# Kernel tuning notes

Hardware: AMD Instinct MI355X
Metric: run time of the kernel (lower is better)

## Reference

```python
import jax, jax.numpy as jnp
import numpy as np

H = 16  # n_heads

def setup_inputs() -> dict:
    key = jax.random.key(0)
    ks = jax.random.split(key, 12)
    B, L, S, D = 4, 2048, 2048, 1024
    E = D // H  # d_keys = d_values = 64
    s = 1.0 / np.sqrt(D)
    inp = {
        "queries": jax.random.normal(ks[0], (B, L, D), jnp.float32),
        "keys": jax.random.normal(ks[1], (B, S, D), jnp.float32),
        "values": jax.random.normal(ks[2], (B, S, D), jnp.float32),
        # causal boolean mask: True = masked out
        "attn_mask": jnp.triu(jnp.ones((L, S), jnp.bool_), k=1)[None, None],
        "Wq": jax.random.normal(ks[3], (H * E, D), jnp.float32) * s,
        "bq": jnp.zeros((H * E,), jnp.float32),
        "Wk": jax.random.normal(ks[4], (H * E, D), jnp.float32) * s,
        "bk": jnp.zeros((H * E,), jnp.float32),
        "Wv": jax.random.normal(ks[5], (H * E, D), jnp.float32) * s,
        "bv": jnp.zeros((H * E,), jnp.float32),
        "Wo": jax.random.normal(ks[6], (D, H * E), jnp.float32) * s,
        "bo": jnp.zeros((D,), jnp.float32),
    }
    return inp


def reference(queries, keys, values, attn_mask, Wq, bq, Wk, bk, Wv, bv, Wo, bo):
    B, L, D = queries.shape
    S = keys.shape[1]
    E = Wq.shape[0] // H
    # QKV projections + head split: (B, L/S, H, E)
    q = (queries @ Wq.T + bq).reshape(B, L, H, E)
    k = (keys @ Wk.T + bk).reshape(B, S, H, E)
    v = (values @ Wv.T + bv).reshape(B, S, H, E)
    scale = 1.0 / jnp.sqrt(jnp.asarray(E, q.dtype))
    scores = jnp.einsum("blhe,bshe->bhls", q, k) * scale  # (B,H,L,S)
    scores = jnp.where(attn_mask, jnp.asarray(-jnp.inf, scores.dtype), scores)
    A = jax.nn.softmax(scores, axis=-1)
    out = jnp.einsum("bhls,bshe->blhe", A, v).reshape(B, L, H * E)
    return out @ Wo.T + bo
```

## Files before the change

### kernel.cpp

```cpp
#include <hip/hip_runtime.h>
#include <hip/hip_bf16.h>

typedef float f32x4 __attribute__((ext_vector_type(4)));
typedef short s16x8 __attribute__((ext_vector_type(8)));
typedef short s16x4 __attribute__((ext_vector_type(4)));
typedef unsigned short u16;

#define H_ 16
#define E_ 64
#define D_ 1024
#define L_ 2048
#define NQT 32
#define SCL2E 0.18033688011f

__device__ __forceinline__ u16 f2bf(float f) {
  union { float f; unsigned u; } v; v.f = f;
  unsigned u = v.u;
  u += 0x7fffu + ((u >> 16) & 1u);
  return (u16)(u >> 16);
}

__device__ __forceinline__ unsigned pkbf(float a, float b) {
  unsigned r;
  asm("v_cvt_pk_bf16_f32 %0, %1, %2" : "=v"(r) : "v"(a), "v"(b));
  return r;
}

__device__ __forceinline__ void gld16(const u16* g, u16* l) {
  __builtin_amdgcn_global_load_lds((const __attribute__((address_space(1))) void*)g,
                                   (__attribute__((address_space(3))) void*)l, 16, 0, 0);
}

__global__ __launch_bounds__(256) void cvtall(const float* __restrict__ q,
                                              const float* __restrict__ k,
                                              const float* __restrict__ v,
                                              const float* __restrict__ w0,
                                              const float* __restrict__ w1,
                                              const float* __restrict__ w2,
                                              const float* __restrict__ w3,
                                              u16* __restrict__ qd,
                                              u16* __restrict__ kd,
                                              u16* __restrict__ vd,
                                              u16* __restrict__ d0,
                                              u16* __restrict__ d1,
                                              u16* __restrict__ d2,
                                              u16* __restrict__ d3) {
  const int b = blockIdx.x;
  const float* src; u16* dst; float s = 1.0f; size_t off;
  if (b < 12288) {
    const int y = b >> 12, bx = b & 4095;
    src = y == 0 ? q : (y == 1 ? k : v);
    dst = y == 0 ? qd : (y == 1 ? kd : vd);
    off = ((size_t)bx * 256 + threadIdx.x) * 8;
  } else {
    const int b2 = b - 12288, y = b2 >> 9, bx = b2 & 511;
    src = y == 0 ? w0 : (y == 1 ? w1 : (y == 2 ? w2 : w3));
    dst = y == 0 ? d0 : (y == 1 ? d1 : (y == 2 ? d2 : d3));
    if (y == 0) s = SCL2E;
    off = ((size_t)bx * 256 + threadIdx.x) * 8;
  }
  const f32x4 a = *(const f32x4*)(src + off);
  const f32x4 c = *(const f32x4*)(src + off + 4);
  s16x8 r;
#pragma unroll
  for (int j = 0; j < 4; ++j) { r[j] = (short)f2bf(a[j] * s); r[j + 4] = (short)f2bf(c[j] * s); }
  *(s16x8*)(dst + off) = r;
}

template<int PERMUTE>
__global__ __launch_bounds__(256) void gemm_lds(const u16* __restrict__ A,
                                                const u16* __restrict__ W,
                                                const float* __restrict__ bias,
                                                void* __restrict__ outp,
                                                int M, int N, int K, float bsc)
{
  __shared__ __align__(16) u16 As[2][128][64];
  __shared__ __align__(16) u16 Bs[2][128][64];
  const int tid = threadIdx.x;
  const int m0 = blockIdx.y * 128, n0 = blockIdx.x * 128;
  const int w = tid >> 6, lane = tid & 63, g = lane >> 4, li = lane & 15;
  const int wr = w >> 1, wc = w & 1;

  int sOff[4];
#pragma unroll
  for (int j = 0; j < 4; ++j) {
    const int s = (w * 4 + j) * 64 + lane;
    const int row = s >> 3, c8 = s & 7;
    sOff[j] = row * K + ((c8 ^ (row & 7)) * 8);
  }

  f32x4 acc[4][4];
#pragma unroll
  for (int i = 0; i < 4; ++i)
#pragma unroll
    for (int j = 0; j < 4; ++j) acc[i][j] = (f32x4){0.f, 0.f, 0.f, 0.f};

  const u16* Abase = A + (size_t)m0 * K;
  const u16* Wbase = W + (size_t)n0 * K;
  const int swz = li & 7;

  auto STAGE = [&](int k0, int bf) {
#pragma unroll
    for (int j = 0; j < 4; ++j) {
      gld16(Abase + k0 + sOff[j], &As[bf][(w * 4 + j) * 8][0]);
      gld16(Wbase + k0 + sOff[j], &Bs[bf][(w * 4 + j) * 8][0]);
    }
  };

  STAGE(0, 0);
  __syncthreads();
  int buf = 0;
  for (int k0 = 0; k0 < K; k0 += 64) {
    if (k0 + 64 < K) STAGE(k0 + 64, buf ^ 1);

    s16x8 a[2][4], b[2][4];
#pragma unroll
    for (int kk = 0; kk < 2; ++kk) {
      const int cg = ((kk * 4 + g) ^ swz) * 8;
#pragma unroll
      for (int mi = 0; mi < 4; ++mi) a[kk][mi] = *(const s16x8*)&As[buf][wr * 64 + mi * 16 + li][cg];
#pragma unroll
      for (int ni = 0; ni < 4; ++ni) b[kk][ni] = *(const s16x8*)&Bs[buf][wc * 64 + ni * 16 + li][cg];
    }
#pragma unroll
    for (int kk = 0; kk < 2; ++kk)
#pragma unroll
      for (int mi = 0; mi < 4; ++mi)
#pragma unroll
        for (int ni = 0; ni < 4; ++ni)
          acc[mi][ni] = __builtin_amdgcn_mfma_f32_16x16x32_bf16(a[kk][mi], b[kk][ni], acc[mi][ni], 0, 0, 0);

    __syncthreads();
    buf ^= 1;
  }

#pragma unroll
  for (int mi = 0; mi < 4; ++mi) {
#pragma unroll
    for (int ni = 0; ni < 4; ++ni) {
      const int row = m0 + wr * 64 + mi * 16 + g * 4;
      const int col = n0 + wc * 64 + ni * 16 + li;
      const float bv = bias[col] * bsc;
      if (PERMUTE == 2) {
        s16x4 pk;
#pragma unroll
        for (int r = 0; r < 4; ++r) pk[r] = (short)f2bf(acc[mi][ni][r] + bv);
        const int bb = row >> 11, lq = row & (L_ - 1);
        const int hh = col >> 6, e = col & (E_ - 1);
        *(s16x4*)&((u16*)outp)[(((size_t)bb * H_ + hh) * E_ + e) * L_ + lq] = pk;
      } else {
#pragma unroll
        for (int r = 0; r < 4; ++r) {
          const float v = acc[mi][ni][r] + bv;
          const int rr = row + r;
          if (PERMUTE == 1) {
            const int bb = rr >> 11, lq = rr & (L_ - 1);
            const int hh = col >> 6, e = col & (E_ - 1);
            ((u16*)outp)[(((size_t)bb * H_ + hh) * L_ + lq) * E_ + e] = f2bf(v);
          } else {
            ((float*)outp)[(size_t)rr * N + col] = v;
          }
        }
      }
    }
  }
}

template<int A_BF16, int PERMUTE>
__global__ __launch_bounds__(256) void gemm_bt(const void* __restrict__ Aptr,
                                               const float* __restrict__ W,
                                               const float* __restrict__ bias,
                                               void* __restrict__ outp,
                                               int M, int N, int K, float osc)
{
  __shared__ __align__(16) short As[2][128][40];
  __shared__ __align__(16) short Bs[2][128][40];
  const int tid = threadIdx.x;
  const int m0 = blockIdx.y * 128, n0 = blockIdx.x * 128;
  const int w = tid >> 6, lane = tid & 63, g = lane >> 4, li = lane & 15;
  const int wr = w >> 1, wc = w & 1;

  f32x4 acc[4][4];
#pragma unroll
  for (int i = 0; i < 4; ++i)
#pragma unroll
    for (int j = 0; j < 4; ++j) acc[i][j] = (f32x4){0.f, 0.f, 0.f, 0.f};

  f32x4 ra0[2], ra1[2];
  s16x8 rab[2];
  f32x4 rb0[2], rb1[2];

  auto LOAD = [&](int k0) {
#pragma unroll
    for (int p = 0; p < 2; ++p) {
      const int c = p * 256 + tid, row = c >> 2, kc = (c & 3) * 8;
      if (A_BF16) {
        rab[p] = *(const s16x8*)((const u16*)Aptr + (size_t)(m0 + row) * K + k0 + kc);
      } else {
        const float* ap = (const float*)Aptr + (size_t)(m0 + row) * K + k0 + kc;
        ra0[p] = *(const f32x4*)ap; ra1[p] = *(const f32x4*)(ap + 4);
      }
      const float* wp = W + (size_t)(n0 + row) * K + k0 + kc;
      rb0[p] = *(const f32x4*)wp; rb1[p] = *(const f32x4*)(wp + 4);
    }
  };
  auto WRITE = [&](int buf) {
#pragma unroll
    for (int p = 0; p < 2; ++p) {
      const int c = p * 256 + tid, row = c >> 2, kc = (c & 3) * 8;
      if (A_BF16) {
        *(s16x8*)&As[buf][row][kc] = rab[p];
      } else {
        s16x8 r;
#pragma unroll
        for (int j = 0; j < 4; ++j) { r[j] = (short)f2bf(ra0[p][j]); r[j + 4] = (short)f2bf(ra1[p][j]); }
        *(s16x8*)&As[buf][row][kc] = r;
      }
      s16x8 rb;
#pragma unroll
      for (int j = 0; j < 4; ++j) { rb[j] = (short)f2bf(rb0[p][j]); rb[j + 4] = (short)f2bf(rb1[p][j]); }
      *(s16x8*)&Bs[buf][row][kc] = rb;
    }
  };

  LOAD(0); WRITE(0);
  __syncthreads();
  int cur = 0;
  for (int k0 = 0; k0 < K; k0 += 32) {
    const bool more = (k0 + 32 < K);
    if (more) LOAD(k0 + 32);

    s16x8 a[4], b[4];
#pragma unroll
    for (int mi = 0; mi < 4; ++mi) a[mi] = *(const s16x8*)&As[cur][wr * 64 + mi * 16 + li][g * 8];
#pragma unroll
    for (int ni = 0; ni < 4; ++ni) b[ni] = *(const s16x8*)&Bs[cur][wc * 64 + ni * 16 + li][g * 8];
#pragma unroll
    for (int mi = 0; mi < 4; ++mi)
#pragma unroll
      for (int ni = 0; ni < 4; ++ni)
        acc[mi][ni] = __builtin_amdgcn_mfma_f32_16x16x32_bf16(a[mi], b[ni], acc[mi][ni], 0, 0, 0);

    if (more) { WRITE(cur ^ 1); __syncthreads(); }
    cur ^= 1;
  }

#pragma unroll
  for (int mi = 0; mi < 4; ++mi) {
#pragma unroll
    for (int ni = 0; ni < 4; ++ni) {
      const int row = m0 + wr * 64 + mi * 16 + g * 4;
      const int col = n0 + wc * 64 + ni * 16 + li;
      const float bv = bias[col];
      if (PERMUTE == 2) {
        s16x4 pk;
#pragma unroll
        for (int r = 0; r < 4; ++r) pk[r] = (short)f2bf((acc[mi][ni][r] + bv) * osc);
        const int bb = row >> 11, lq = row & (L_ - 1);
        const int hh = col >> 6, e = col & (E_ - 1);
        *(s16x4*)&((u16*)outp)[(((size_t)bb * H_ + hh) * E_ + e) * L_ + lq] = pk;
      } else {
#pragma unroll
        for (int r = 0; r < 4; ++r) {
          const float v = (acc[mi][ni][r] + bv) * osc;
          const int rr = row + r;
          if (PERMUTE == 1) {
            const int bb = rr >> 11, lq = rr & (L_ - 1);
            const int hh = col >> 6, e = col & (E_ - 1);
            ((u16*)outp)[(((size_t)bb * H_ + hh) * L_ + lq) * E_ + e] = f2bf(v);
          } else {
            ((float*)outp)[(size_t)rr * N + col] = v;
          }
        }
      }
    }
  }
}

__global__ __launch_bounds__(256) void attn_kernel(const u16* __restrict__ qp,
                                                   const u16* __restrict__ kp,
                                                   const u16* __restrict__ vtp,
                                                   u16* __restrict__ op)
{
  __shared__ __align__(16) u16 Ks[2][4096];
  __shared__ __align__(16) u16 Vs[2][4096];
  const int tid = threadIdx.x;
  const unsigned wgid = blockIdx.x;
  const int bh = (wgid & 7) * 8 + ((wgid >> 3) & 7);
  const int qb = NQT - 1 - (int)(wgid >> 6);
  const int w = tid >> 6, lane = tid & 63, g = lane >> 4, li = lane & 15;
  const size_t base  = (size_t)bh * L_ * E_;
  const size_t baseT = (size_t)bh * E_ * L_;
  const int bb = bh >> 4, hh = bh & 15;
  const int qbase = qb * 64;

  const u16* qr = qp + base + (size_t)(qbase + w * 16 + li) * E_;
  const s16x8 qa0 = *(const s16x8*)(qr + g * 8);
  const s16x8 qa1 = *(const s16x8*)(qr + 32 + g * 8);

  f32x4 o[4];
  float m_run = -1e30f, l_run = 0.f;
#pragma unroll
  for (int nc = 0; nc < 4; ++nc) o[nc] = (f32x4){0.f, 0.f, 0.f, 0.f};

  int kSrc[2], vSrc[2];
#pragma unroll
  for (int j = 0; j < 2; ++j) {
    const int s = (w * 2 + j) * 64 + lane;
    const int row = s >> 3;
    const int c8 = (s & 7) ^ ((row & 3) | (((row >> 3) & 1) << 2));
    kSrc[j] = row * E_ + c8 * 8;
    vSrc[j] = row * L_ + c8 * 8;
  }
  auto stage = [&](int t, int buf) {
    const int kvb = t * 64;
#pragma unroll
    for (int j = 0; j < 2; ++j) {
      gld16(kp + base + (size_t)kvb * E_ + kSrc[j], &Ks[buf][(w * 2 + j) * 512]);
      gld16(vtp + baseT + kvb + vSrc[j],            &Vs[buf][(w * 2 + j) * 512]);
    }
  };

  const int swzk = li & 7;
  const int swzv = (li & 3) | (((li >> 3) & 1) << 2);
  int kRd[8], vRd[8];
#pragma unroll
  for (int inst = 0; inst < 4; ++inst) {
    const int bs = (32 * (inst >> 1) + 4 * (inst & 1) + 8 * (li >> 2) + (li & 3)) * 8;
    kRd[inst * 2]     = (bs + (g ^ swzk)) * 8;
    kRd[inst * 2 + 1] = (bs + ((g + 4) ^ swzk)) * 8;
  }
#pragma unroll
  for (int nc = 0; nc < 4; ++nc) {
    const int es = (nc * 16 + li) * 8;
    vRd[nc * 2]     = (es + (g ^ swzv)) * 8;
    vRd[nc * 2 + 1] = (es + ((g + 4) ^ swzv)) * 8;
  }

  stage(0, 0);
  __syncthreads();
  int buf = 0;
  for (int t = 0; t <= qb; ++t) {
    const bool more = (t < qb);
    if (more) stage(t + 1, buf ^ 1);

    s16x8 kf[8];
#pragma unroll
    for (int i = 0; i < 8; ++i) kf[i] = *(const s16x8*)&Ks[buf][kRd[i]];
    f32x4 p[4];
#pragma unroll
    for (int inst = 0; inst < 4; ++inst) {
      f32x4 sf = (f32x4){0.f, 0.f, 0.f, 0.f};
      sf = __builtin_amdgcn_mfma_f32_16x16x32_bf16(kf[inst * 2],     qa0, sf, 0, 0, 0);
      sf = __builtin_amdgcn_mfma_f32_16x16x32_bf16(kf[inst * 2 + 1], qa1, sf, 0, 0, 0);
      p[inst] = sf;
    }
    if (t == qb) {
      const int qrow = qbase + w * 16 + li;
      const int kvb = t * 64;
#pragma unroll
      for (int inst = 0; inst < 4; ++inst)
#pragma unroll
        for (int r = 0; r < 4; ++r)
          if (kvb + 32 * (inst >> 1) + 8 * g + 4 * (inst & 1) + r > qrow) p[inst][r] = -1e30f;
    }

    s16x8 vf[8];
#pragma unroll
    for (int i = 0; i < 8; ++i) vf[i] = *(const s16x8*)&Vs[buf][vRd[i]];

    {
      float m0_ = fmaxf(fmaxf(p[0][0], p[0][1]), fmaxf(p[0][2], p[0][3]));
      float m1_ = fmaxf(fmaxf(p[1][0], p[1][1]), fmaxf(p[1][2], p[1][3]));
      float m2_ = fmaxf(fmaxf(p[2][0], p[2][1]), fmaxf(p[2][2], p[2][3]));
      float m3_ = fmaxf(fmaxf(p[3][0], p[3][1]), fmaxf(p[3][2], p[3][3]));
      const float mx16 = fmaxf(fmaxf(m0_, m1_), fmaxf(m2_, m3_));
      if (__any(mx16 > m_run + 8.0f)) {
        float mx = fmaxf(mx16, __shfl_xor(mx16, 16));
        mx = fmaxf(mx, __shfl_xor(mx, 32));
        const float mn = fmaxf(m_run, mx);
        const float alpha = __builtin_amdgcn_exp2f(m_run - mn);
        m_run = mn;
        l_run *= alpha;
#pragma unroll
        for (int nc = 0; nc < 4; ++nc)
#pragma unroll
          for (int r = 0; r < 4; ++r) o[nc][r] *= alpha;
      }
    }
    unsigned pk[8];
    float rs = 0.f;
#pragma unroll
    for (int inst = 0; inst < 4; ++inst) {
      const float e0 = __builtin_amdgcn_exp2f(p[inst][0] - m_run);
      const float e1 = __builtin_amdgcn_exp2f(p[inst][1] - m_run);
      const float e2 = __builtin_amdgcn_exp2f(p[inst][2] - m_run);
      const float e3 = __builtin_amdgcn_exp2f(p[inst][3] - m_run);
      rs += (e0 + e1) + (e2 + e3);
      pk[inst * 2]     = pkbf(e0, e1);
      pk[inst * 2 + 1] = pkbf(e2, e3);
    }
    l_run += rs;

    union { s16x8 v; unsigned u[4]; } A0, A1;
    A0.u[0] = pk[0]; A0.u[1] = pk[1]; A0.u[2] = pk[2]; A0.u[3] = pk[3];
    A1.u[0] = pk[4]; A1.u[1] = pk[5]; A1.u[2] = pk[6]; A1.u[3] = pk[7];
#pragma unroll
    for (int nc = 0; nc < 4; ++nc) {
      o[nc] = __builtin_amdgcn_mfma_f32_16x16x32_bf16(vf[nc * 2],     A0.v, o[nc], 0, 0, 0);
      o[nc] = __builtin_amdgcn_mfma_f32_16x16x32_bf16(vf[nc * 2 + 1], A1.v, o[nc], 0, 0, 0);
    }

    if (more) __syncthreads();
    buf ^= 1;
  }

  float lsum = l_run;
  lsum += __shfl_xor(lsum, 16);
  lsum += __shfl_xor(lsum, 32);
  const float inv = 1.0f / lsum;
  u16* orow = op + ((size_t)bb * L_ + qbase + w * 16 + li) * D_ + hh * E_;
#pragma unroll
  for (int nc = 0; nc < 4; ++nc) {
    union { s16x4 v; unsigned u[2]; } P;
    P.u[0] = pkbf(o[nc][0] * inv, o[nc][1] * inv);
    P.u[1] = pkbf(o[nc][2] * inv, o[nc][3] * inv);
    *(s16x4*)&orow[nc * 16 + g * 4] = P.v;
  }
}

extern "C" void kernel_launch(void* const* d_in, const int* in_sizes, int n_in,
                              void* d_out, int out_size, void* d_ws, size_t ws_size,
                              hipStream_t stream) {
  const float* queries = (const float*)d_in[0];
  const float* keys    = (const float*)d_in[1];
  const float* values  = (const float*)d_in[2];
  const float* Wq = (const float*)d_in[4];
  const float* bq = (const float*)d_in[5];
  const float* Wk = (const float*)d_in[6];
  const float* bk = (const float*)d_in[7];
  const float* Wv = (const float*)d_in[8];
  const float* bv = (const float*)d_in[9];
  const float* Wo = (const float*)d_in[10];
  const float* bo = (const float*)d_in[11];

  const size_t MD = (size_t)8192 * 1024;
  const size_t WN = (size_t)1024 * 1024;
  u16* qbuf = (u16*)d_ws;
  u16* kbuf = qbuf + MD;
  u16* vbuf = kbuf + MD;
  u16* abuf = vbuf + MD;

  dim3 blk(256);
  dim3 ggrid(8, 64);

  const size_t need = (4 * MD + 4 * WN) * sizeof(u16);
  if (ws_size >= need) {
    u16* qcv = abuf;
    u16* kcv = qbuf;
    u16* vcv = kbuf;
    u16* wqb = abuf + MD;
    u16* wkb = wqb + WN;
    u16* wvb = wkb + WN;
    u16* wob = wvb + WN;

    cvtall<<<dim3(14336), blk, 0, stream>>>(queries, keys, values, Wq, Wk, Wv, Wo,
                                            qcv, kcv, vcv, wqb, wkb, wvb, wob);

    gemm_lds<2><<<ggrid, blk, 0, stream>>>(vcv, wvb, bv, vbuf, 8192, 1024, 1024, 1.0f);
    gemm_lds<1><<<ggrid, blk, 0, stream>>>(kcv, wkb, bk, kbuf, 8192, 1024, 1024, 1.0f);
    gemm_lds<1><<<ggrid, blk, 0, stream>>>(qcv, wqb, bq, qbuf, 8192, 1024, 1024, SCL2E);
    attn_kernel<<<dim3(2048), blk, 0, stream>>>(qbuf, kbuf, vbuf, abuf);
    gemm_lds<0><<<ggrid, blk, 0, stream>>>(abuf, wob, bo, d_out, 8192, 1024, 1024, 1.0f);
  } else {
    gemm_bt<0, 1><<<ggrid, blk, 0, stream>>>(queries, Wq, bq, qbuf, 8192, 1024, 1024, SCL2E);
    gemm_bt<0, 1><<<ggrid, blk, 0, stream>>>(keys,    Wk, bk, kbuf, 8192, 1024, 1024, 1.0f);
    gemm_bt<0, 2><<<ggrid, blk, 0, stream>>>(values,  Wv, bv, vbuf, 8192, 1024, 1024, 1.0f);
    attn_kernel<<<dim3(2048), blk, 0, stream>>>(qbuf, kbuf, vbuf, abuf);
    gemm_bt<1, 0><<<ggrid, blk, 0, stream>>>(abuf, Wo, bo, d_out, 8192, 1024, 1024, 1.0f);
  }
}
```

Measured before the change: 186.5 us.

## Enlarge attention query tile to 128 rows with 8 waves per block

The attention kernel now processes 128 query rows per workgroup using 512 threads (8 waves) instead of 64 rows with 4 waves, halving the grid to 1024 blocks. Each K/V tile staged into LDS is shared by twice as many query rows, which cuts global K/V traffic and staging per query. Each thread now issues one async load per tile instead of two, and the causal masking branch covers the last two KV tiles. The cost is fewer, larger blocks, so occupancy and load balance across the causal triangle may suffer. The diagonal blocks also do some extra masked work.

```diff
diff --git a/kernel.cpp b/kernel.cpp
--- a/kernel.cpp
+++ b/kernel.cpp
@@ -10,7 +10,6 @@
 #define E_ 64
 #define D_ 1024
 #define L_ 2048
-#define NQT 32
 #define SCL2E 0.18033688011f
 
 __device__ __forceinline__ u16 f2bf(float f) {
@@ -277,7 +276,7 @@
   }
 }
 
-__global__ __launch_bounds__(256) void attn_kernel(const u16* __restrict__ qp,
+__global__ __launch_bounds__(512) void attn_kernel(const u16* __restrict__ qp,
                                                    const u16* __restrict__ kp,
                                                    const u16* __restrict__ vtp,
                                                    u16* __restrict__ op)
@@ -287,12 +286,13 @@
   const int tid = threadIdx.x;
   const unsigned wgid = blockIdx.x;
   const int bh = (wgid & 7) * 8 + ((wgid >> 3) & 7);
-  const int qb = NQT - 1 - (int)(wgid >> 6);
+  const int qb = 15 - (int)(wgid >> 6);
   const int w = tid >> 6, lane = tid & 63, g = lane >> 4, li = lane & 15;
   const size_t base  = (size_t)bh * L_ * E_;
   const size_t baseT = (size_t)bh * E_ * L_;
   const int bb = bh >> 4, hh = bh & 15;
-  const int qbase = qb * 64;
+  const int qbase = qb * 128;
+  const int nt = 2 * qb + 2;
 
   const u16* qr = qp + base + (size_t)(qbase + w * 16 + li) * E_;
   const s16x8 qa0 = *(const s16x8*)(qr + g * 8);
@@ -303,22 +303,18 @@
 #pragma unroll
   for (int nc = 0; nc < 4; ++nc) o[nc] = (f32x4){0.f, 0.f, 0.f, 0.f};
 
-  int kSrc[2], vSrc[2];
-#pragma unroll
-  for (int j = 0; j < 2; ++j) {
-    const int s = (w * 2 + j) * 64 + lane;
+  int kSrc, vSrc;
+  {
+    const int s = w * 64 + lane;
     const int row = s >> 3;
     const int c8 = (s & 7) ^ ((row & 3) | (((row >> 3) & 1) << 2));
-    kSrc[j] = row * E_ + c8 * 8;
-    vSrc[j] = row * L_ + c8 * 8;
+    kSrc = row * E_ + c8 * 8;
+    vSrc = row * L_ + c8 * 8;
   }
   auto stage = [&](int t, int buf) {
     const int kvb = t * 64;
-#pragma unroll
-    for (int j = 0; j < 2; ++j) {
-      gld16(kp + base + (size_t)kvb * E_ + kSrc[j], &Ks[buf][(w * 2 + j) * 512]);
-      gld16(vtp + baseT + kvb + vSrc[j],            &Vs[buf][(w * 2 + j) * 512]);
-    }
+    gld16(kp + base + (size_t)kvb * E_ + kSrc, &Ks[buf][w * 512]);
+    gld16(vtp + baseT + kvb + vSrc,            &Vs[buf][w * 512]);
   };
 
   const int swzk = li & 7;
@@ -340,8 +336,8 @@
   stage(0, 0);
   __syncthreads();
   int buf = 0;
-  for (int t = 0; t <= qb; ++t) {
-    const bool more = (t < qb);
+  for (int t = 0; t < nt; ++t) {
+    const bool more = (t + 1 < nt);
     if (more) stage(t + 1, buf ^ 1);
 
     s16x8 kf[8];
@@ -355,7 +351,7 @@
       sf = __builtin_amdgcn_mfma_f32_16x16x32_bf16(kf[inst * 2 + 1], qa1, sf, 0, 0, 0);
       p[inst] = sf;
     }
-    if (t == qb) {
+    if (t >= 2 * qb) {
       const int qrow = qbase + w * 16 + li;
       const int kvb = t * 64;
 #pragma unroll
@@ -470,13 +466,13 @@
     gemm_lds<2><<<ggrid, blk, 0, stream>>>(vcv, wvb, bv, vbuf, 8192, 1024, 1024, 1.0f);
     gemm_lds<1><<<ggrid, blk, 0, stream>>>(kcv, wkb, bk, kbuf, 8192, 1024, 1024, 1.0f);
     gemm_lds<1><<<ggrid, blk, 0, stream>>>(qcv, wqb, bq, qbuf, 8192, 1024, 1024, SCL2E);
-    attn_kernel<<<dim3(2048), blk, 0, stream>>>(qbuf, kbuf, vbuf, abuf);
+    attn_kernel<<<dim3(1024), dim3(512), 0, stream>>>(qbuf, kbuf, vbuf, abuf);
     gemm_lds<0><<<ggrid, blk, 0, stream>>>(abuf, wob, bo, d_out, 8192, 1024, 1024, 1.0f);
   } else {
     gemm_bt<0, 1><<<ggrid, blk, 0, stream>>>(queries, Wq, bq, qbuf, 8192, 1024, 1024, SCL2E);
     gemm_bt<0, 1><<<ggrid, blk, 0, stream>>>(keys,    Wk, bk, kbuf, 8192, 1024, 1024, 1.0f);
     gemm_bt<0, 2><<<ggrid, blk, 0, stream>>>(values,  Wv, bv, vbuf, 8192, 1024, 1024, 1.0f);
-    attn_kernel<<<dim3(2048), blk, 0, stream>>>(qbuf, kbuf, vbuf, abuf);
+    attn_kernel<<<dim3(1024), dim3(512), 0, stream>>>(qbuf, kbuf, vbuf, abuf);
     gemm_bt<1, 0><<<ggrid, blk, 0, stream>>>(abuf, Wo, bo, d_out, 8192, 1024, 1024, 1.0f);
   }
 }
```

New measurement: 185.5 us. Within noise of the previous version (-0.6%).

## Process 128 query rows per attention block, two 16-row slices per wave

Applied to the files above, without the earlier changes.

The attention kernel now gives each workgroup a 128-row query tile instead of 64. Each wave handles two 16-row query slices that share every K/V tile loaded into LDS, and the grid shrinks from 2048 to 1024 blocks. This halves K/V global traffic and LDS staging per query row. In exchange it doubles the accumulator registers per wave, masks two diagonal tiles instead of one, and leaves fewer blocks to balance the causal work across CUs.

```diff
diff --git a/kernel.cpp b/kernel.cpp
--- a/kernel.cpp
+++ b/kernel.cpp
@@ -10,7 +10,6 @@
 #define E_ 64
 #define D_ 1024
 #define L_ 2048
-#define NQT 32
 #define SCL2E 0.18033688011f
 
 __device__ __forceinline__ u16 f2bf(float f) {
@@ -287,21 +286,27 @@
   const int tid = threadIdx.x;
   const unsigned wgid = blockIdx.x;
   const int bh = (wgid & 7) * 8 + ((wgid >> 3) & 7);
-  const int qb = NQT - 1 - (int)(wgid >> 6);
+  const int qb = 15 - (int)(wgid >> 6);
   const int w = tid >> 6, lane = tid & 63, g = lane >> 4, li = lane & 15;
   const size_t base  = (size_t)bh * L_ * E_;
   const size_t baseT = (size_t)bh * E_ * L_;
   const int bb = bh >> 4, hh = bh & 15;
-  const int qbase = qb * 64;
-
-  const u16* qr = qp + base + (size_t)(qbase + w * 16 + li) * E_;
-  const s16x8 qa0 = *(const s16x8*)(qr + g * 8);
-  const s16x8 qa1 = *(const s16x8*)(qr + 32 + g * 8);
-
-  f32x4 o[4];
-  float m_run = -1e30f, l_run = 0.f;
-#pragma unroll
-  for (int nc = 0; nc < 4; ++nc) o[nc] = (f32x4){0.f, 0.f, 0.f, 0.f};
+  const int qbase = qb * 128;
+  const int nt = 2 * qb + 2;
+  const int rowA = qbase + w * 32 + li;
+  const int rowB = rowA + 16;
+
+  const u16* qrA = qp + base + (size_t)rowA * E_;
+  const s16x8 qaA0 = *(const s16x8*)(qrA + g * 8);
+  const s16x8 qaA1 = *(const s16x8*)(qrA + 32 + g * 8);
+  const u16* qrB = qp + base + (size_t)rowB * E_;
+  const s16x8 qaB0 = *(const s16x8*)(qrB + g * 8);
+  const s16x8 qaB1 = *(const s16x8*)(qrB + 32 + g * 8);
+
+  f32x4 oA[4], oB[4];
+  float mA = -1e30f, lA = 0.f, mB = -1e30f, lB = 0.f;
+#pragma unroll
+  for (int nc = 0; nc < 4; ++nc) { oA[nc] = (f32x4){0.f,0.f,0.f,0.f}; oB[nc] = (f32x4){0.f,0.f,0.f,0.f}; }
 
   int kSrc[2], vSrc[2];
 #pragma unroll
@@ -337,26 +342,18 @@
     vRd[nc * 2 + 1] = (es + ((g + 4) ^ swzv)) * 8;
   }
 
-  stage(0, 0);
-  __syncthreads();
-  int buf = 0;
-  for (int t = 0; t <= qb; ++t) {
-    const bool more = (t < qb);
-    if (more) stage(t + 1, buf ^ 1);
-
-    s16x8 kf[8];
-#pragma unroll
-    for (int i = 0; i < 8; ++i) kf[i] = *(const s16x8*)&Ks[buf][kRd[i]];
+  auto half = [&](const s16x8* kf, const s16x8* vf, int t,
+                  const s16x8& q0, const s16x8& q1, int qrow,
+                  f32x4* o, float& m_run, float& l_run) {
     f32x4 p[4];
 #pragma unroll
     for (int inst = 0; inst < 4; ++inst) {
       f32x4 sf = (f32x4){0.f, 0.f, 0.f, 0.f};
-      sf = __builtin_amdgcn_mfma_f32_16x16x32_bf16(kf[inst * 2],     qa0, sf, 0, 0, 0);
-      sf = __builtin_amdgcn_mfma_f32_16x16x32_bf16(kf[inst * 2 + 1], qa1, sf, 0, 0, 0);
+      sf = __builtin_amdgcn_mfma_f32_16x16x32_bf16(kf[inst * 2],     q0, sf, 0, 0, 0);
+      sf = __builtin_amdgcn_mfma_f32_16x16x32_bf16(kf[inst * 2 + 1], q1, sf, 0, 0, 0);
       p[inst] = sf;
     }
-    if (t == qb) {
-      const int qrow = qbase + w * 16 + li;
+    if (t >= 2 * qb) {
       const int kvb = t * 64;
 #pragma unroll
       for (int inst = 0; inst < 4; ++inst)
@@ -364,11 +361,6 @@
         for (int r = 0; r < 4; ++r)
           if (kvb + 32 * (inst >> 1) + 8 * g + 4 * (inst & 1) + r > qrow) p[inst][r] = -1e30f;
     }
-
-    s16x8 vf[8];
-#pragma unroll
-    for (int i = 0; i < 8; ++i) vf[i] = *(const s16x8*)&Vs[buf][vRd[i]];
-
     {
       float m0_ = fmaxf(fmaxf(p[0][0], p[0][1]), fmaxf(p[0][2], p[0][3]));
       float m1_ = fmaxf(fmaxf(p[1][0], p[1][1]), fmaxf(p[1][2], p[1][3]));
@@ -401,7 +393,6 @@
       pk[inst * 2 + 1] = pkbf(e2, e3);
     }
     l_run += rs;
-
     union { s16x8 v; unsigned u[4]; } A0, A1;
     A0.u[0] = pk[0]; A0.u[1] = pk[1]; A0.u[2] = pk[2]; A0.u[3] = pk[3];
     A1.u[0] = pk[4]; A1.u[1] = pk[5]; A1.u[2] = pk[6]; A1.u[3] = pk[7];
@@ -410,23 +401,44 @@
       o[nc] = __builtin_amdgcn_mfma_f32_16x16x32_bf16(vf[nc * 2],     A0.v, o[nc], 0, 0, 0);
       o[nc] = __builtin_amdgcn_mfma_f32_16x16x32_bf16(vf[nc * 2 + 1], A1.v, o[nc], 0, 0, 0);
     }
+  };
+
+  stage(0, 0);
+  __syncthreads();
+  int buf = 0;
+  for (int t = 0; t < nt; ++t) {
+    const bool more = (t + 1 < nt);
+    if (more) stage(t + 1, buf ^ 1);
+
+    s16x8 kf[8], vf[8];
+#pragma unroll
+    for (int i = 0; i < 8; ++i) kf[i] = *(const s16x8*)&Ks[buf][kRd[i]];
+#pragma unroll
+    for (int i = 0; i < 8; ++i) vf[i] = *(const s16x8*)&Vs[buf][vRd[i]];
+
+    half(kf, vf, t, qaA0, qaA1, rowA, oA, mA, lA);
+    half(kf, vf, t, qaB0, qaB1, rowB, oB, mB, lB);
 
     if (more) __syncthreads();
     buf ^= 1;
   }
 
-  float lsum = l_run;
-  lsum += __shfl_xor(lsum, 16);
-  lsum += __shfl_xor(lsum, 32);
-  const float inv = 1.0f / lsum;
-  u16* orow = op + ((size_t)bb * L_ + qbase + w * 16 + li) * D_ + hh * E_;
-#pragma unroll
-  for (int nc = 0; nc < 4; ++nc) {
-    union { s16x4 v; unsigned u[2]; } P;
-    P.u[0] = pkbf(o[nc][0] * inv, o[nc][1] * inv);
-    P.u[1] = pkbf(o[nc][2] * inv, o[nc][3] * inv);
-    *(s16x4*)&orow[nc * 16 + g * 4] = P.v;
-  }
+  auto epi = [&](const f32x4* o, float l_run, int qrow) {
+    float lsum = l_run;
+    lsum += __shfl_xor(lsum, 16);
+    lsum += __shfl_xor(lsum, 32);
+    const float inv = 1.0f / lsum;
+    u16* orow = op + ((size_t)bb * L_ + qrow) * D_ + hh * E_;
+#pragma unroll
+    for (int nc = 0; nc < 4; ++nc) {
+      union { s16x4 v; unsigned u[2]; } P;
+      P.u[0] = pkbf(o[nc][0] * inv, o[nc][1] * inv);
+      P.u[1] = pkbf(o[nc][2] * inv, o[nc][3] * inv);
+      *(s16x4*)&orow[nc * 16 + g * 4] = P.v;
+    }
+  };
+  epi(oA, lA, rowA);
+  epi(oB, lB, rowB);
 }
 
 extern "C" void kernel_launch(void* const* d_in, const int* in_sizes, int n_in,
@@ -470,13 +482,13 @@
     gemm_lds<2><<<ggrid, blk, 0, stream>>>(vcv, wvb, bv, vbuf, 8192, 1024, 1024, 1.0f);
     gemm_lds<1><<<ggrid, blk, 0, stream>>>(kcv, wkb, bk, kbuf, 8192, 1024, 1024, 1.0f);
     gemm_lds<1><<<ggrid, blk, 0, stream>>>(qcv, wqb, bq, qbuf, 8192, 1024, 1024, SCL2E);
-    attn_kernel<<<dim3(2048), blk, 0, stream>>>(qbuf, kbuf, vbuf, abuf);
+    attn_kernel<<<dim3(1024), blk, 0, stream>>>(qbuf, kbuf, vbuf, abuf);
     gemm_lds<0><<<ggrid, blk, 0, stream>>>(abuf, wob, bo, d_out, 8192, 1024, 1024, 1.0f);
   } else {
     gemm_bt<0, 1><<<ggrid, blk, 0, stream>>>(queries, Wq, bq, qbuf, 8192, 1024, 1024, SCL2E);
     gemm_bt<0, 1><<<ggrid, blk, 0, stream>>>(keys,    Wk, bk, kbuf, 8192, 1024, 1024, 1.0f);
     gemm_bt<0, 2><<<ggrid, blk, 0, stream>>>(values,  Wv, bv, vbuf, 8192, 1024, 1024, 1.0f);
-    attn_kernel<<<dim3(2048), blk, 0, stream>>>(qbuf, kbuf, vbuf, abuf);
+    attn_kernel<<<dim3(1024), blk, 0, stream>>>(qbuf, kbuf, vbuf, abuf);
     gemm_bt<1, 0><<<ggrid, blk, 0, stream>>>(abuf, Wo, bo, d_out, 8192, 1024, 1024, 1.0f);
   }
 }
```

Result: slower. 197.3 us (+5.8%).
